# Optimization experiments

Measured on AMD Instinct MI355X. Metric: run time of the kernel, lower is better.

The kernel has to match this reference:

```python
import jax, jax.numpy as jnp
import numpy as np

B, C, W, H = 4, 64, 64, 64
CH = 64  # ch == input_nc so residual is valid

def setup_inputs() -> dict:
    key = jax.random.key(0)
    ks = jax.random.split(key, 5)
    return {
        "x": jax.random.normal(ks[0], (B, C, W, H), jnp.float32),
        "y": jax.random.normal(ks[1], (B, C, W, H), jnp.float32),
        "Wf": jax.random.normal(ks[2], (CH // 2, C), jnp.float32) * 0.05,
        "bf": jnp.zeros((CH // 2,), jnp.float32),
        "Wg": jax.random.normal(ks[3], (CH // 2, C), jnp.float32) * 0.05,
        "bg": jnp.zeros((CH // 2,), jnp.float32),
        "Wh": jax.random.normal(ks[4], (CH, C), jnp.float32) * 0.05,
        "bh": jnp.zeros((CH,), jnp.float32),
        "gamma": jnp.full((1,), 0.5, jnp.float32),
    }

def reference(x, y, Wf, bf, Wg, bg, Wh, bh, gamma):
    b, c, w, h = x.shape
    n = w * h
    xf = x.reshape(b, c, n)   # [b, C, N]
    yf = y.reshape(b, c, n)
    # 1x1 convs == per-pixel linear maps over channels
    f = jnp.einsum('oc,bcn->bon', Wf, xf) + bf[None, :, None]   # [b, CH/2, N]
    g = jnp.einsum('oc,bcn->bon', Wg, yf) + bg[None, :, None]   # [b, CH/2, N]
    hv = jnp.einsum('oc,bcn->bon', Wh, yf) + bh[None, :, None]  # [b, CH,   N]
    # s = g^T @ f : [b, N, N]
    s = jnp.einsum('bcm,bcn->bmn', g, f)
    beta = jax.nn.softmax(s, axis=-1)
    # o = beta @ h^T : [b, N, CH]
    o = jnp.einsum('bmn,bcn->bmc', beta, hv)
    o = o.transpose(0, 2, 1).reshape(b, -1, w, h)  # [b, CH, w, h]
    return gamma[0] * o + x
```

## Files before the change

kernel.cpp:

```cpp
#include <hip/hip_runtime.h>
#include <hip/hip_bf16.h>

#define BB  4
#define CC  64
#define NN  4096
#define CF  32
#define CHN 64

typedef __attribute__((ext_vector_type(8)))  __bf16 bf16x8;
typedef __attribute__((ext_vector_type(4)))  __bf16 bf16x4;
typedef __attribute__((ext_vector_type(4)))  float  floatx4;
typedef __attribute__((ext_vector_type(16))) float  floatx16;
typedef __attribute__((ext_vector_type(2)))  unsigned int uintx2;
typedef __attribute__((ext_vector_type(4)))  unsigned int uintx4;

__device__ __forceinline__ float scrub(float v) {
    return fminf(fmaxf(v, -1e30f), 1e30f);
}

__device__ __forceinline__ unsigned cvt_pk_bf16(float lo, float hi) {
    unsigned r;
    asm("v_cvt_pk_bf16_f32 %0, %1, %2" : "=v"(r) : "v"(lo), "v"(hi));
    return r;
}

__global__ __launch_bounds__(256) void prep_kernel(
    const float* __restrict__ x, const float* __restrict__ y,
    const float* __restrict__ Wf, const float* __restrict__ bfp,
    const float* __restrict__ Wg, const float* __restrict__ bgp,
    const float* __restrict__ Wh, const float* __restrict__ bhp,
    __bf16* __restrict__ fT, __bf16* __restrict__ gT, __bf16* __restrict__ hvb)
{
    __shared__ __align__(16) __bf16 wbf[128][72];
    __shared__ float sbias[128];

    const int t  = threadIdx.x;
    const int w  = t >> 6;
    const int l  = t & 63;
    const int lo = l & 15;
    const int q  = l >> 4;

    const int b   = blockIdx.x >> 6;
    const int nb  = blockIdx.x & 63;
    const int nn  = nb * 64 + w * 16 + lo;

    for (int i = t; i < 128 * CC; i += 256) {
        int row = i >> 6, c = i & 63;
        float wv;
        if (row < 32)      wv = Wf[(size_t)row * CC + c];
        else if (row < 64) wv = Wg[(size_t)(row - 32) * CC + c];
        else               wv = Wh[(size_t)(row - 64) * CC + c];
        wbf[row][c] = (__bf16)wv;
    }
    if (t < 128) {
        if (t < 32)      sbias[t] = bfp[t];
        else if (t < 64) sbias[t] = bgp[t - 32];
        else             sbias[t] = bhp[t - 64];
    }
    __syncthreads();

    const float* xb = x + (size_t)b * CC * NN;
    const float* yb = y + (size_t)b * CC * NN;
    bf16x8 bx[2], by[2];
    #pragma unroll
    for (int kh = 0; kh < 2; kh++) {
        #pragma unroll
        for (int j = 0; j < 8; j++) {
            int c = kh * 32 + q * 8 + j;
            bx[kh][j] = (__bf16)xb[(size_t)c * NN + nn];
            by[kh][j] = (__bf16)yb[(size_t)c * NN + nn];
        }
    }

    const floatx4 zero4 = {0.f, 0.f, 0.f, 0.f};
    #pragma unroll
    for (int ct = 0; ct < 8; ct++) {
        const bf16x8* src = (ct < 2) ? bx : by;
        floatx4 acc = zero4;
        #pragma unroll
        for (int kh = 0; kh < 2; kh++) {
            const bf16x8 a = *(const bf16x8*)&wbf[ct*16 + lo][kh*32 + q*8];
            acc = __builtin_amdgcn_mfma_f32_16x16x32_bf16(a, src[kh], acc, 0, 0, 0);
        }
        if (ct < 4) {
            bf16x4 pk;
            #pragma unroll
            for (int r = 0; r < 4; r++)
                pk[r] = (__bf16)(acc[r] + sbias[ct*16 + q*4 + r]);
            __bf16* dstbase = (ct < 2) ? fT : gT;
            int cho = (ct & 1) * 16;
            *(bf16x4*)&dstbase[((size_t)b * NN + nn) * CF + cho + q*4] = pk;
        } else {
            #pragma unroll
            for (int r = 0; r < 4; r++) {
                int ch = (ct - 4) * 16 + q*4 + r;
                hvb[((size_t)b * CHN + ch) * NN + nn] =
                    (__bf16)(acc[r] + sbias[64 + ch]);
            }
        }
    }
}

__global__ __launch_bounds__(512, 2) void attn_kernel(
    const __bf16* __restrict__ fT, const __bf16* __restrict__ gT,
    const __bf16* __restrict__ hvb,
    const float* __restrict__ x, const float* __restrict__ gamma_p,
    float* __restrict__ out)
{
    __shared__ float osum[8][64][67];
    __shared__ float lsum[512];

    const int t   = threadIdx.x;
    const int w   = t >> 6;
    const int l   = t & 63;
    const int l31 = l & 31;
    const int hi  = l >> 5;

    const int slot = blockIdx.x;
    const int xcd  = slot & 7;
    const int b    = xcd >> 1;
    const int mg   = ((xcd & 1) << 5) | (slot >> 3);
    const int m0   = mg * 64;

    const __bf16* fb = fT  + (size_t)b * NN * CF;
    const __bf16* gb = gT  + (size_t)b * NN * CF;
    const __bf16* hb = hvb + (size_t)b * CHN * NN;

    bf16x8 bg_[2][2];
    #pragma unroll
    for (int mt = 0; mt < 2; mt++)
        #pragma unroll
        for (int kk = 0; kk < 2; kk++)
            bg_[mt][kk] = *(const bf16x8*)(gb + (size_t)(m0 + mt*32 + l31) * CF + kk*16 + hi*8);

    const floatx16 zero16 = {};
    floatx16 oacc[2][2];
    #pragma unroll
    for (int mt = 0; mt < 2; mt++)
        #pragma unroll
        for (int ct = 0; ct < 2; ct++) oacc[mt][ct] = zero16;
    float rsum[2] = {0.f, 0.f};

    for (int i = 0; i < 8; i++) {
        const int n0 = (8*i + w) * 64;

        bf16x8 af[2][2];
        #pragma unroll
        for (int nt = 0; nt < 2; nt++)
            #pragma unroll
            for (int kk = 0; kk < 2; kk++)
                af[nt][kk] = *(const bf16x8*)(fb + (size_t)(n0 + nt*32 + l31) * CF + kk*16 + hi*8);

        bf16x8 bv[2][4];
        #pragma unroll
        for (int ct = 0; ct < 2; ct++)
            #pragma unroll
            for (int ks = 0; ks < 4; ks++)
                bv[ct][ks] = *(const bf16x8*)(hb + (size_t)(ct*32 + l31) * NN + n0 + ks*16 + hi*8);

        bf16x8 pa[2][4];
        #pragma unroll
        for (int mt = 0; mt < 2; mt++) {
            #pragma unroll
            for (int nt = 0; nt < 2; nt++) {
                floatx16 s = __builtin_amdgcn_mfma_f32_32x32x16_bf16(
                    af[nt][0], bg_[mt][0], zero16, 0, 0, 0);
                s = __builtin_amdgcn_mfma_f32_32x32x16_bf16(
                    af[nt][1], bg_[mt][1], s, 0, 0, 0);

                float p[16];
                #pragma unroll
                for (int r = 0; r < 16; r++) p[r] = __expf(s[r]);

                unsigned W[8];
                #pragma unroll
                for (int g = 0; g < 8; g++) W[g] = cvt_pk_bf16(p[2*g], p[2*g+1]);

                #pragma unroll
                for (int g = 0; g < 8; g++)
                    rsum[mt] += __uint_as_float(W[g] << 16)
                              + __uint_as_float(W[g] & 0xffff0000u);

                uintx2 s02 = __builtin_amdgcn_permlane32_swap(W[0], W[2], false, false);
                uintx2 s13 = __builtin_amdgcn_permlane32_swap(W[1], W[3], false, false);
                uintx2 s46 = __builtin_amdgcn_permlane32_swap(W[4], W[6], false, false);
                uintx2 s57 = __builtin_amdgcn_permlane32_swap(W[5], W[7], false, false);

                uintx4 w0 = {s02.x, s13.x, s02.y, s13.y};
                uintx4 w1 = {s46.x, s57.x, s46.y, s57.y};
                pa[mt][nt*2 + 0] = __builtin_bit_cast(bf16x8, w0);
                pa[mt][nt*2 + 1] = __builtin_bit_cast(bf16x8, w1);
            }
        }

        #pragma unroll
        for (int mt = 0; mt < 2; mt++)
            #pragma unroll
            for (int ct = 0; ct < 2; ct++)
                #pragma unroll
                for (int ks = 0; ks < 4; ks++)
                    oacc[mt][ct] = __builtin_amdgcn_mfma_f32_32x32x16_bf16(
                        pa[mt][ks], bv[ct][ks], oacc[mt][ct], 0, 0, 0);
    }

    #pragma unroll
    for (int mt = 0; mt < 2; mt++)
        rsum[mt] += __shfl_xor(rsum[mt], 32, 64);

    #pragma unroll
    for (int mt = 0; mt < 2; mt++) {
        #pragma unroll
        for (int ct = 0; ct < 2; ct++)
            #pragma unroll
            for (int r = 0; r < 16; r++)
                osum[w][mt*32 + ((r&3) + 8*(r>>2) + 4*hi)][ct*32 + l31] =
                    oacc[mt][ct][r];
        if (hi == 0)
            lsum[w*64 + mt*32 + l31] = rsum[mt];
    }
    __syncthreads();

    const float gam = gamma_p[0];
    const int m  = t & 63;
    const int cb = t >> 6;
    float lt = 0.f;
    #pragma unroll
    for (int s = 0; s < 8; s++) lt += lsum[s*64 + m];
    const float inv = 1.f / lt;
    #pragma unroll
    for (int it = 0; it < 8; it++) {
        const int ch = it*8 + cb;
        float acc = 0.f;
        #pragma unroll
        for (int s = 0; s < 8; s++) acc += osum[s][m][ch];
        size_t gi = ((size_t)b * CHN + ch) * NN + m0 + m;
        float ov = scrub(acc * inv);
        out[gi] = gam * ov + x[gi];
    }
}

extern "C" void kernel_launch(void* const* d_in, const int* in_sizes, int n_in,
                              void* d_out, int out_size, void* d_ws, size_t ws_size,
                              hipStream_t stream)
{
    const float* x     = (const float*)d_in[0];
    const float* y     = (const float*)d_in[1];
    const float* Wf    = (const float*)d_in[2];
    const float* bf    = (const float*)d_in[3];
    const float* Wg    = (const float*)d_in[4];
    const float* bg    = (const float*)d_in[5];
    const float* Wh    = (const float*)d_in[6];
    const float* bh    = (const float*)d_in[7];
    const float* gamma = (const float*)d_in[8];
    float* out = (float*)d_out;

    __bf16* wsb = (__bf16*)d_ws;
    __bf16* fT  = wsb;
    __bf16* gT  = fT + (size_t)BB * NN * CF;
    __bf16* hvb = gT + (size_t)BB * NN * CF;

    prep_kernel<<<dim3(BB * 64), dim3(256), 0, stream>>>(
        x, y, Wf, bf, Wg, bg, Wh, bh, fT, gT, hvb);
    attn_kernel<<<dim3(BB * 64), dim3(512), 0, stream>>>(
        fT, gT, hvb, x, gamma, out);
}
```

Before: 102.3 us.

## Tile f/g/h buffers into MFMA-native blocks and split attention output channels across blocks

The prep kernel now writes fT, gT and hv in a blocked layout matching the 32x32x16 MFMA operand pattern, so each lane's 16-byte loads are contiguous. The attention kernel's work split also changes. Each block now handles 128 query rows for one half of the 64 output channels, instead of 64 rows for all channels. This halves the V operand traffic per block and changes the shape of the shared-memory reduction. In exchange, the QK^T MFMAs and the exp work per query row are done twice, once in each channel-half block.

Result: slower. 108.5 us (+6.1%).

```diff
diff --git a/kernel.cpp b/kernel.cpp
--- a/kernel.cpp
+++ b/kernel.cpp
@@ -23,6 +23,7 @@
     asm("v_cvt_pk_bf16_f32 %0, %1, %2" : "=v"(r) : "v"(lo), "v"(hi));
     return r;
 }
+
 
 __global__ __launch_bounds__(256) void prep_kernel(
     const float* __restrict__ x, const float* __restrict__ y,
@@ -88,13 +89,18 @@
             for (int r = 0; r < 4; r++)
                 pk[r] = (__bf16)(acc[r] + sbias[ct*16 + q*4 + r]);
             __bf16* dstbase = (ct < 2) ? fT : gT;
-            int cho = (ct & 1) * 16;
-            *(bf16x4*)&dstbase[((size_t)b * NN + nn) * CF + cho + q*4] = pk;
+            const int c0 = (ct & 1) * 16 + q * 4;
+            const int off = (nn >> 5)*1024 + (c0 >> 4)*512 + (nn & 31)*16
+                          + ((c0 >> 3) & 1)*8 + (c0 & 7);
+            *(bf16x4*)&dstbase[(size_t)b * NN * CF + off] = pk;
         } else {
             #pragma unroll
             for (int r = 0; r < 4; r++) {
                 int ch = (ct - 4) * 16 + q*4 + r;
-                hvb[((size_t)b * CHN + ch) * NN + nn] =
+                const int off = (nn >> 6)*4096 + (ch >> 5)*2048
+                              + ((nn >> 4) & 3)*512 + (ch & 31)*16
+                              + ((nn >> 3) & 1)*8 + (nn & 7);
+                hvb[(size_t)b * CHN * NN + off] =
                     (__bf16)(acc[r] + sbias[64 + ch]);
             }
         }
@@ -107,8 +113,8 @@
     const float* __restrict__ x, const float* __restrict__ gamma_p,
     float* __restrict__ out)
 {
-    __shared__ float osum[8][64][67];
-    __shared__ float lsum[512];
+    __shared__ float osum[8][128][33];
+    __shared__ float lsum[1024];
 
     const int t   = threadIdx.x;
     const int w   = t >> 6;
@@ -119,48 +125,47 @@
     const int slot = blockIdx.x;
     const int xcd  = slot & 7;
     const int b    = xcd >> 1;
-    const int mg   = ((xcd & 1) << 5) | (slot >> 3);
-    const int m0   = mg * 64;
+    const int chh  = xcd & 1;
+    const int mg   = slot >> 3;
+    const int m0   = mg * 128;
 
     const __bf16* fb = fT  + (size_t)b * NN * CF;
     const __bf16* gb = gT  + (size_t)b * NN * CF;
     const __bf16* hb = hvb + (size_t)b * CHN * NN;
 
-    bf16x8 bg_[2][2];
-    #pragma unroll
-    for (int mt = 0; mt < 2; mt++)
+    const int lane16 = (l31 * 2 + hi) * 8;
+
+    bf16x8 bg_[4][2];
+    #pragma unroll
+    for (int mt = 0; mt < 4; mt++)
         #pragma unroll
         for (int kk = 0; kk < 2; kk++)
-            bg_[mt][kk] = *(const bf16x8*)(gb + (size_t)(m0 + mt*32 + l31) * CF + kk*16 + hi*8);
+            bg_[mt][kk] = *(const bf16x8*)(gb + (size_t)(mg*4 + mt)*1024 + kk*512 + lane16);
 
     const floatx16 zero16 = {};
-    floatx16 oacc[2][2];
-    #pragma unroll
-    for (int mt = 0; mt < 2; mt++)
-        #pragma unroll
-        for (int ct = 0; ct < 2; ct++) oacc[mt][ct] = zero16;
-    float rsum[2] = {0.f, 0.f};
+    floatx16 oacc[4];
+    #pragma unroll
+    for (int mt = 0; mt < 4; mt++) oacc[mt] = zero16;
+    float rsum[4] = {0.f, 0.f, 0.f, 0.f};
 
     for (int i = 0; i < 8; i++) {
-        const int n0 = (8*i + w) * 64;
+        const int nc = 8*i + w;
 
         bf16x8 af[2][2];
         #pragma unroll
         for (int nt = 0; nt < 2; nt++)
             #pragma unroll
             for (int kk = 0; kk < 2; kk++)
-                af[nt][kk] = *(const bf16x8*)(fb + (size_t)(n0 + nt*32 + l31) * CF + kk*16 + hi*8);
-
-        bf16x8 bv[2][4];
-        #pragma unroll
-        for (int ct = 0; ct < 2; ct++)
-            #pragma unroll
-            for (int ks = 0; ks < 4; ks++)
-                bv[ct][ks] = *(const bf16x8*)(hb + (size_t)(ct*32 + l31) * NN + n0 + ks*16 + hi*8);
-
-        bf16x8 pa[2][4];
-        #pragma unroll
-        for (int mt = 0; mt < 2; mt++) {
+                af[nt][kk] = *(const bf16x8*)(fb + (size_t)(nc*2 + nt)*1024 + kk*512 + lane16);
+
+        bf16x8 bv[4];
+        #pragma unroll
+        for (int ks = 0; ks < 4; ks++)
+            bv[ks] = *(const bf16x8*)(hb + (size_t)nc*4096 + chh*2048 + ks*512 + lane16);
+
+        #pragma unroll
+        for (int mt = 0; mt < 4; mt++) {
+            bf16x8 pa[4];
             #pragma unroll
             for (int nt = 0; nt < 2; nt++) {
                 floatx16 s = __builtin_amdgcn_mfma_f32_32x32x16_bf16(
@@ -188,51 +193,44 @@
 
                 uintx4 w0 = {s02.x, s13.x, s02.y, s13.y};
                 uintx4 w1 = {s46.x, s57.x, s46.y, s57.y};
-                pa[mt][nt*2 + 0] = __builtin_bit_cast(bf16x8, w0);
-                pa[mt][nt*2 + 1] = __builtin_bit_cast(bf16x8, w1);
+                pa[nt*2 + 0] = __builtin_bit_cast(bf16x8, w0);
+                pa[nt*2 + 1] = __builtin_bit_cast(bf16x8, w1);
             }
-        }
-
-        #pragma unroll
-        for (int mt = 0; mt < 2; mt++)
-            #pragma unroll
-            for (int ct = 0; ct < 2; ct++)
-                #pragma unroll
-                for (int ks = 0; ks < 4; ks++)
-                    oacc[mt][ct] = __builtin_amdgcn_mfma_f32_32x32x16_bf16(
-                        pa[mt][ks], bv[ct][ks], oacc[mt][ct], 0, 0, 0);
-    }
-
-    #pragma unroll
-    for (int mt = 0; mt < 2; mt++)
+            #pragma unroll
+            for (int ks = 0; ks < 4; ks++)
+                oacc[mt] = __builtin_amdgcn_mfma_f32_32x32x16_bf16(
+                    pa[ks], bv[ks], oacc[mt], 0, 0, 0);
+        }
+    }
+
+    #pragma unroll
+    for (int mt = 0; mt < 4; mt++)
         rsum[mt] += __shfl_xor(rsum[mt], 32, 64);
 
     #pragma unroll
-    for (int mt = 0; mt < 2; mt++) {
-        #pragma unroll
-        for (int ct = 0; ct < 2; ct++)
-            #pragma unroll
-            for (int r = 0; r < 16; r++)
-                osum[w][mt*32 + ((r&3) + 8*(r>>2) + 4*hi)][ct*32 + l31] =
-                    oacc[mt][ct][r];
+    for (int mt = 0; mt < 4; mt++) {
+        #pragma unroll
+        for (int r = 0; r < 16; r++)
+            osum[w][mt*32 + ((r&3) + 8*(r>>2) + 4*hi)][l31] = oacc[mt][r];
         if (hi == 0)
-            lsum[w*64 + mt*32 + l31] = rsum[mt];
+            lsum[w*128 + mt*32 + l31] = rsum[mt];
     }
     __syncthreads();
 
     const float gam = gamma_p[0];
-    const int m  = t & 63;
-    const int cb = t >> 6;
+    const int m  = t & 127;
+    const int cb = t >> 7;
     float lt = 0.f;
     #pragma unroll
-    for (int s = 0; s < 8; s++) lt += lsum[s*64 + m];
+    for (int s = 0; s < 8; s++) lt += lsum[s*128 + m];
     const float inv = 1.f / lt;
     #pragma unroll
     for (int it = 0; it < 8; it++) {
-        const int ch = it*8 + cb;
+        const int chl = it*4 + cb;
+        const int ch  = chh*32 + chl;
         float acc = 0.f;
         #pragma unroll
-        for (int s = 0; s < 8; s++) acc += osum[s][m][ch];
+        for (int s = 0; s < 8; s++) acc += osum[s][m][chl];
         size_t gi = ((size_t)b * CHN + ch) * NN + m0 + m;
         float ov = scrub(acc * inv);
         out[gi] = gam * ov + x[gi];
```
